# Optimization experiments

Hardware: AMD Instinct MI355X
Metric: run time of the kernel (lower is better)

Reference implementation:

```python
import jax, jax.numpy as jnp
import numpy as np

B, T, E, D, OUT = 512, 128, 256, 256, 1  # batch, steps, enc_hidden, dec_hidden, out_feats


def setup_inputs() -> dict:
    key = jax.random.key(0)
    ks = jax.random.split(key, 16)
    s = lambda k, sh, sc=0.05: jax.random.normal(k, sh, dtype=jnp.float32) * sc
    return {
        "input_encoded": jax.random.normal(ks[0], (B, T, E), dtype=jnp.float32),
        "y_history": jax.random.normal(ks[1], (B, T), dtype=jnp.float32),
        # attn_layer: Linear(2D+E -> E), Tanh, Linear(E -> 1)
        "attn_w1": s(ks[2], (2 * D + E, E)),
        "attn_b1": s(ks[3], (E,)),
        "attn_w2": s(ks[4], (E, 1)),
        "attn_b2": s(ks[5], (1,)),
        # LSTM(out_feats -> D), PyTorch gate order i,f,g,o
        "lstm_w_ih": s(ks[6], (4 * D, OUT)),
        "lstm_w_hh": s(ks[7], (4 * D, D)),
        "lstm_b_ih": s(ks[8], (4 * D,)),
        "lstm_b_hh": s(ks[9], (4 * D,)),
        # fc: Linear(E + out_feats -> out_feats), weight init normal_() in torch
        "fc_w": jax.random.normal(ks[10], (E + OUT, OUT), dtype=jnp.float32),
        "fc_b": s(ks[11], (OUT,)),
        # fc_final: Linear(D + E -> out_feats)
        "fcf_w": s(ks[12], (D + E, OUT)),
        "fcf_b": s(ks[13], (OUT,)),
    }


def _decoder(input_encoded, y_history, attn_w1, attn_b1, attn_w2, attn_b2,
             lstm_w_ih, lstm_w_hh, lstm_b_ih, lstm_b_hh, fc_w, fc_b, fcf_w, fcf_b):
    b, t_steps, e = input_encoded.shape
    d = lstm_w_hh.shape[1]

    def step(carry, y_t):
        h, c, _ = carry  # h,c: [B,D]
        # additive attention over encoder timesteps
        hc = jnp.concatenate([h, c], axis=-1)                      # [B,2D]
        hc_rep = jnp.broadcast_to(hc[:, None, :], (b, t_steps, 2 * d))
        x = jnp.concatenate([hc_rep, input_encoded], axis=-1)      # [B,T,2D+E]
        scores = jnp.tanh(x @ attn_w1 + attn_b1) @ attn_w2 + attn_b2  # [B,T,1]
        attn = jax.nn.softmax(scores[..., 0], axis=1)              # [B,T]
        ctx = jnp.einsum('bt,bte->be', attn, input_encoded)        # [B,E]
        # project (context, y_t) to LSTM input
        y_tilde = jnp.concatenate([ctx, y_t[:, None]], axis=-1) @ fc_w + fc_b  # [B,OUT]
        # one LSTM cell step (gate order i,f,g,o)
        gates = y_tilde @ lstm_w_ih.T + lstm_b_ih + h @ lstm_w_hh.T + lstm_b_hh  # [B,4D]
        i_g, f_g, g_g, o_g = jnp.split(gates, 4, axis=-1)
        c_new = jax.nn.sigmoid(f_g) * c + jax.nn.sigmoid(i_g) * jnp.tanh(g_g)
        h_new = jax.nn.sigmoid(o_g) * jnp.tanh(c_new)
        return (h_new, c_new, ctx), None

    init = (jnp.zeros((b, d), jnp.float32), jnp.zeros((b, d), jnp.float32),
            jnp.zeros((b, e), jnp.float32))
    (h, c, ctx), _ = jax.lax.scan(step, init, y_history.T)  # scan over T
    return jnp.concatenate([h, ctx], axis=-1) @ fcf_w + fcf_b  # [B,OUT]


def reference(input_encoded, y_history, attn_w1, attn_b1, attn_w2, attn_b2,
              lstm_w_ih, lstm_w_hh, lstm_b_ih, lstm_b_hh, fc_w, fc_b, fcf_w, fcf_b):
    return _decoder(input_encoded, y_history, attn_w1, attn_b1, attn_w2, attn_b2,
                    lstm_w_ih, lstm_w_hh, lstm_b_ih, lstm_b_hh, fc_w, fc_b, fcf_w, fcf_b)
```

## Files before the change

### kernel.cpp

```cpp
#include <hip/hip_runtime.h>
#include <hip/hip_bf16.h>

#define NT 128
#define NE 256
#define ND 256

__device__ __forceinline__ float fast_tanh(float x) {
    const float e = __expf(2.f * x);
    return __builtin_fmaf(-2.f, __fdividef(1.f, e + 1.f), 1.f);
}
__device__ __forceinline__ float fast_sigm(float x) {
    return __fdividef(1.f, 1.f + __expf(-x));
}
__device__ __forceinline__ void fma4(float4& a, float s, const float4 b) {
    a.x += s * b.x; a.y += s * b.y; a.z += s * b.z; a.w += s * b.w;
}
__device__ __forceinline__ unsigned short f2bf(float f) {
    unsigned int u = __float_as_uint(f);
    return (unsigned short)((u + 0x7FFFu + ((u >> 16) & 1u)) >> 16);
}
__device__ __forceinline__ float4 unpk(uint2 u) {
    float4 r;
    r.x = __uint_as_float(u.x << 16);
    r.y = __uint_as_float(u.x & 0xFFFF0000u);
    r.z = __uint_as_float(u.y << 16);
    r.w = __uint_as_float(u.y & 0xFFFF0000u);
    return r;
}
__device__ __forceinline__ uint2 pk4(float4 v) {
    uint2 u;
    u.x = (unsigned int)f2bf(v.x) | ((unsigned int)f2bf(v.y) << 16);
    u.y = (unsigned int)f2bf(v.z) | ((unsigned int)f2bf(v.w) << 16);
    return u;
}

__global__ __launch_bounds__(256) void prep_w1_bias(
    const float* __restrict__ w1, const float* __restrict__ bih,
    const float* __restrict__ bhh, unsigned short* __restrict__ w1bf,
    float* __restrict__ biasg)
{
    const int t = threadIdx.x, blk = blockIdx.x;
    if (blk < 512) {
        const int idx = blk * 256 + t;
        w1bf[idx] = f2bf(w1[idx]);
    } else {
        for (int g = t; g < 1024; g += 256) biasg[g] = bih[g] + bhh[g];
    }
}

__global__ __launch_bounds__(256) void transpose_whh_bf(
    const float* __restrict__ whh, unsigned short* __restrict__ whhT)
{
    __shared__ float tile[64][65];
    const int t = threadIdx.x;
    const int bi = blockIdx.x >> 2;
    const int bj = blockIdx.x & 3;
    #pragma unroll
    for (int k = 0; k < 16; ++k) {
        const int idx = k * 256 + t, r = idx >> 6, c = idx & 63;
        tile[r][c] = whh[(size_t)(bi * 64 + r) * 256 + bj * 64 + c];
    }
    __syncthreads();
    #pragma unroll
    for (int k = 0; k < 16; ++k) {
        const int idx = k * 256 + t, r = idx >> 6, c = idx & 63;
        whhT[(size_t)(bj * 64 + r) * 1024 + bi * 64 + c] = f2bf(tile[c][r]);
    }
}

__global__ __launch_bounds__(256) void pre_enc_kernel(
    const float* __restrict__ enc, const float* __restrict__ w1,
    const float* __restrict__ b1, unsigned short* __restrict__ prebf)
{
    __shared__ __align__(16) float encs[8][256];
    const int t = threadIdx.x;
    const size_t r0 = (size_t)blockIdx.x * 8;
    for (int k = t; k < 512; k += 256) {
        const int rl = k >> 6, i4 = (k & 63) * 4;
        *(float4*)&encs[rl][i4] = *(const float4*)(enc + (r0 + rl) * 256 + i4);
    }
    __syncthreads();
    const int rl = t >> 5;
    const int j0 = (t & 31) * 8;
    float4 a0 = *(const float4*)(b1 + j0);
    float4 a1 = *(const float4*)(b1 + j0 + 4);
    const float* wp = w1 + (size_t)512 * 256 + j0;
    #pragma unroll 2
    for (int i = 0; i < 256; i += 4) {
        const float4 e4 = *(const float4*)&encs[rl][i];
        const float* w_i = wp + (size_t)i * 256;
        float4 wa, wb;
        wa = *(const float4*)(w_i);        wb = *(const float4*)(w_i + 4);
        fma4(a0, e4.x, wa); fma4(a1, e4.x, wb);
        wa = *(const float4*)(w_i + 256);  wb = *(const float4*)(w_i + 260);
        fma4(a0, e4.y, wa); fma4(a1, e4.y, wb);
        wa = *(const float4*)(w_i + 512);  wb = *(const float4*)(w_i + 516);
        fma4(a0, e4.z, wa); fma4(a1, e4.z, wb);
        wa = *(const float4*)(w_i + 768);  wb = *(const float4*)(w_i + 772);
        fma4(a0, e4.w, wa); fma4(a1, e4.w, wb);
    }
    unsigned short* op = prebf + (r0 + rl) * 256 + j0;
    const uint2 u0 = pk4(a0), u1 = pk4(a1);
    *(uint2*)op = u0;
    *(uint2*)(op + 4) = u1;
}

__global__ __launch_bounds__(1024) void decoder_main(
    const float* __restrict__ enc, const float* __restrict__ yhist,
    const unsigned short* __restrict__ prebf,
    const unsigned short* __restrict__ w1bf,
    const float* __restrict__ w2g, const unsigned short* __restrict__ whhT,
    const float* __restrict__ wih, const float* __restrict__ biasg,
    const float* __restrict__ fcw, const float* __restrict__ fcb,
    const float* __restrict__ fcfw, const float* __restrict__ fcfb,
    float* __restrict__ out)
{
    __shared__ __align__(16) unsigned short encs[2][128][256];
    __shared__ __align__(16) float part[4096];
    __shared__ __align__(16) float hc2[512][2];
    __shared__ __align__(16) float prehc[2][256];
    __shared__ __align__(16) float scores[2][128];
    __shared__ __align__(16) float ctx[2][256];
    __shared__ __align__(16) float w2s[256];
    __shared__ __align__(16) float fcws[258];
    __shared__ __align__(16) float ys[2][128];
    __shared__ float red[16];
    __shared__ float ytil[2];

    const int t = threadIdx.x;
    const int lane = t & 63;
    const int wv = t >> 6;
    const int b0 = blockIdx.x * 2;

    ((float*)hc2)[t] = 0.f;
    if (t < 256) w2s[t] = w2g[t];
    if (t < 258) fcws[t] = (t < 257) ? fcw[t] : fcb[0];
    if (t < 256) ys[t >> 7][t & 127] = yhist[(size_t)(b0 + (t >> 7)) * NT + (t & 127)];
    #pragma unroll
    for (int k = 0; k < 16; ++k) {
        const int idx = t + k * 1024;
        const int r = idx >> 13, row = (idx >> 6) & 127, eg = idx & 63;
        const float4 v = *(const float4*)(enc + ((size_t)(b0 + r) * NT + row) * NE + eg * 4);
        *(uint2*)&encs[r][row][eg * 4] = pk4(v);
    }
    const int s_ = t >> 3, jc = t & 7;
    const unsigned short* ppre = prebf + ((size_t)b0 * NT + s_) * NE + jc * 4;
    __syncthreads();

    #pragma unroll 1
    for (int ts = 0; ts < NT; ++ts) {
        {
            const int jg = wv & 1;
            const int ib = ((wv >> 1) << 6) + ((lane >> 5) << 5);
            const int jl = (lane & 31) * 4;
            float4 a0 = {0,0,0,0}, a1 = {0,0,0,0};
            const unsigned short* wp = w1bf + (size_t)ib * 256 + jg * 128 + jl;
            #pragma unroll 4
            for (int i = 0; i < 32; ++i) {
                const float4 w4 = unpk(*(const uint2*)(wp + (size_t)i * 256));
                const float2 h2 = *(const float2*)&hc2[ib + i][0];
                fma4(a0, h2.x, w4);
                fma4(a1, h2.y, w4);
            }
            a0.x += __shfl_xor(a0.x, 32); a0.y += __shfl_xor(a0.y, 32);
            a0.z += __shfl_xor(a0.z, 32); a0.w += __shfl_xor(a0.w, 32);
            a1.x += __shfl_xor(a1.x, 32); a1.y += __shfl_xor(a1.y, 32);
            a1.z += __shfl_xor(a1.z, 32); a1.w += __shfl_xor(a1.w, 32);
            if (lane < 32) {
                *(float4*)&part[wv * 256 + jl]       = a0;
                *(float4*)&part[wv * 256 + 128 + jl] = a1;
            }
        }
        __syncthreads();
        if (t < 512) {
            const int r = t >> 8, j = t & 255, jg = j >> 7, jl = j & 127;
            float s = 0.f;
            #pragma unroll
            for (int k = 0; k < 8; ++k) s += part[(2 * k + jg) * 256 + r * 128 + jl];
            prehc[r][j] = s;
        }
        __syncthreads();

        {
            const unsigned short* pp0 = ppre;
            asm volatile("" : "+v"(pp0));
            const unsigned short* pp1 = pp0 + (size_t)NT * NE;
            float a0 = 0.f, a1 = 0.f;
            #pragma unroll
            for (int i = 0; i < 8; ++i) {
                const int j = i * 32 + jc * 4;
                const float4 wv4 = *(const float4*)&w2s[j];
                const float4 h0 = *(const float4*)&prehc[0][j];
                const float4 h1 = *(const float4*)&prehc[1][j];
                const float4 q0 = unpk(*(const uint2*)(pp0 + i * 32));
                const float4 q1 = unpk(*(const uint2*)(pp1 + i * 32));
                a0 += fast_tanh(q0.x + h0.x) * wv4.x + fast_tanh(q0.y + h0.y) * wv4.y
                    + fast_tanh(q0.z + h0.z) * wv4.z + fast_tanh(q0.w + h0.w) * wv4.w;
                a1 += fast_tanh(q1.x + h1.x) * wv4.x + fast_tanh(q1.y + h1.y) * wv4.y
                    + fast_tanh(q1.z + h1.z) * wv4.z + fast_tanh(q1.w + h1.w) * wv4.w;
            }
            a0 += __shfl_xor(a0, 1); a0 += __shfl_xor(a0, 2); a0 += __shfl_xor(a0, 4);
            a1 += __shfl_xor(a1, 1); a1 += __shfl_xor(a1, 2); a1 += __shfl_xor(a1, 4);
            if (jc == 0) { scores[0][s_] = a0; scores[1][s_] = a1; }
        }
        __syncthreads();

        if (t < 128) {
            const int r = t >> 6, l = t & 63;
            const float v0 = scores[r][l], v1 = scores[r][l + 64];
            float m = fmaxf(v0, v1);
            #pragma unroll
            for (int off = 32; off; off >>= 1) m = fmaxf(m, __shfl_xor(m, off));
            const float e0 = __expf(v0 - m), e1 = __expf(v1 - m);
            float sum = e0 + e1;
            #pragma unroll
            for (int off = 32; off; off >>= 1) sum += __shfl_xor(sum, off);
            const float inv = __fdividef(1.f, sum);
            scores[r][l] = e0 * inv;
            scores[r][l + 64] = e1 * inv;
        }
        __syncthreads();

        {
            const int r2 = t >> 9, sl = (t >> 6) & 7, e4 = (t & 63) * 4;
            float4 acc = {0.f, 0.f, 0.f, 0.f};
            #pragma unroll
            for (int q = 0; q < 16; ++q) {
                const float a = scores[r2][sl * 16 + q];
                const uint2 ev = *(const uint2*)&encs[r2][sl * 16 + q][e4];
                fma4(acc, a, unpk(ev));
            }
            *(float4*)&part[(sl * 2 + r2) * 256 + e4] = acc;
        }
        __syncthreads();
        if (t < 512) {
            const int r = t >> 8, e = t & 255;
            float v = 0.f;
            #pragma unroll
            for (int sl2 = 0; sl2 < 8; ++sl2) v += part[(sl2 * 2 + r) * 256 + e];
            ctx[r][e] = v;
            float p = v * fcws[e];
            #pragma unroll
            for (int off = 32; off; off >>= 1) p += __shfl_xor(p, off);
            if (lane == 0) red[wv] = p;
        }
        __syncthreads();

        {
            if (t < 2)
                ytil[t] = red[4 * t] + red[4 * t + 1] + red[4 * t + 2] + red[4 * t + 3]
                        + ys[t][ts] * fcws[256] + fcws[257];
            const int ks = wv >> 3;
            const int cg = wv & 7;
            const int ibase = ks * 128 + (lane >> 5) * 64;
            const int col = cg * 128 + (lane & 31) * 4;
            float4 c0 = {0,0,0,0}, c1 = {0,0,0,0};
            const unsigned short* wp = whhT + (size_t)ibase * 1024 + col;
            #pragma unroll 8
            for (int i = 0; i < 64; ++i) {
                const float4 w4 = unpk(*(const uint2*)(wp + (size_t)i * 1024));
                const float2 h2 = *(const float2*)&hc2[ibase + i][0];
                fma4(c0, h2.x, w4);
                fma4(c1, h2.y, w4);
            }
            c0.x += __shfl_xor(c0.x, 32); c0.y += __shfl_xor(c0.y, 32);
            c0.z += __shfl_xor(c0.z, 32); c0.w += __shfl_xor(c0.w, 32);
            c1.x += __shfl_xor(c1.x, 32); c1.y += __shfl_xor(c1.y, 32);
            c1.z += __shfl_xor(c1.z, 32); c1.w += __shfl_xor(c1.w, 32);
            if (lane < 32) {
                *(float4*)&part[ks * 2048 + col]        = c0;
                *(float4*)&part[ks * 2048 + 1024 + col] = c1;
            }
        }
        __syncthreads();
        if (t < 512) {
            const int r = t >> 8, d = t & 255;
            const float g0 = part[r * 1024 + d]       + part[2048 + r * 1024 + d];
            const float g1 = part[r * 1024 + 256 + d] + part[2048 + r * 1024 + 256 + d];
            const float g2 = part[r * 1024 + 512 + d] + part[2048 + r * 1024 + 512 + d];
            const float g3 = part[r * 1024 + 768 + d] + part[2048 + r * 1024 + 768 + d];
            const float yt = ytil[r];
            const float gi = g0 + yt * wih[d]       + biasg[d];
            const float gf = g1 + yt * wih[256 + d] + biasg[256 + d];
            const float gg = g2 + yt * wih[512 + d] + biasg[512 + d];
            const float go = g3 + yt * wih[768 + d] + biasg[768 + d];
            const float c_old = hc2[256 + d][r];
            const float cn = fast_sigm(gf) * c_old + fast_sigm(gi) * fast_tanh(gg);
            const float hn = fast_sigm(go) * fast_tanh(cn);
            hc2[d][r] = hn;
            hc2[256 + d][r] = cn;
        }
        __syncthreads();
    }

    if (t < 512) {
        const int r = t >> 8, j = t & 255;
        float p = hc2[j][r] * fcfw[j] + ctx[r][j] * fcfw[256 + j];
        #pragma unroll
        for (int off = 32; off; off >>= 1) p += __shfl_xor(p, off);
        if (lane == 0) red[wv] = p;
    }
    __syncthreads();
    if (t < 2)
        out[b0 + t] = red[4 * t] + red[4 * t + 1] + red[4 * t + 2] + red[4 * t + 3] + fcfb[0];
}

extern "C" void kernel_launch(void* const* d_in, const int* in_sizes, int n_in,
                              void* d_out, int out_size, void* d_ws, size_t ws_size,
                              hipStream_t stream) {
    (void)in_sizes; (void)n_in; (void)out_size; (void)ws_size;
    const float* enc   = (const float*)d_in[0];
    const float* yhist = (const float*)d_in[1];
    const float* w1    = (const float*)d_in[2];
    const float* b1    = (const float*)d_in[3];
    const float* w2    = (const float*)d_in[4];
    const float* wih   = (const float*)d_in[6];
    const float* whh   = (const float*)d_in[7];
    const float* bih   = (const float*)d_in[8];
    const float* bhh   = (const float*)d_in[9];
    const float* fcw   = (const float*)d_in[10];
    const float* fcb   = (const float*)d_in[11];
    const float* fcfw  = (const float*)d_in[12];
    const float* fcfb  = (const float*)d_in[13];
    float* out = (float*)d_out;

    unsigned short* prebf = (unsigned short*)d_ws;
    unsigned short* w1bf  = prebf + 16777216;
    unsigned short* whhT  = w1bf + 131072;
    float* biasg = (float*)(whhT + 262144);

    prep_w1_bias<<<513, 256, 0, stream>>>(w1, bih, bhh, w1bf, biasg);
    transpose_whh_bf<<<64, 256, 0, stream>>>(whh, whhT);
    pre_enc_kernel<<<8192, 256, 0, stream>>>(enc, w1, b1, prebf);
    decoder_main<<<256, 1024, 0, stream>>>(enc, yhist, prebf, w1bf, w2, whhT,
                                           wih, biasg, fcw, fcb, fcfw, fcfb, out);
}
```

Measured before the change: 3.718 ms.

## Use bf16 MFMA for per-step hc·W1 and h·Whh matvecs

Replaces the scalar FMA matvecs for the attention hidden-state projection and the LSTM recurrent gates with 16x16x32 bf16 MFMA instructions. Only 2 of the 16 A-matrix rows carry real batch rows; the rest are zeroed. Weights are pre-packed into MFMA fragment layout, and h/c are kept as bf16 in shared memory, with an fp32 copy of c kept for the cell update. This removes the partial-sum reduction pass and one barrier per step. In exchange, most of each MFMA's work is wasted on zero rows, and rounding h/c to bf16 before the matmuls lowers precision.

```diff
diff --git a/kernel.cpp b/kernel.cpp
--- a/kernel.cpp
+++ b/kernel.cpp
@@ -5,6 +5,9 @@
 #define NE 256
 #define ND 256
 
+typedef __attribute__((ext_vector_type(8))) short bf16x8;
+typedef __attribute__((ext_vector_type(4))) float f32x4;
+
 __device__ __forceinline__ float fast_tanh(float x) {
     const float e = __expf(2.f * x);
     return __builtin_fmaf(-2.f, __fdividef(1.f, e + 1.f), 1.f);
@@ -18,6 +21,9 @@
 __device__ __forceinline__ unsigned short f2bf(float f) {
     unsigned int u = __float_as_uint(f);
     return (unsigned short)((u + 0x7FFFu + ((u >> 16) & 1u)) >> 16);
+}
+__device__ __forceinline__ float bf2f(unsigned short s) {
+    return __uint_as_float(((unsigned int)s) << 16);
 }
 __device__ __forceinline__ float4 unpk(uint2 u) {
     float4 r;
@@ -34,37 +40,43 @@
     return u;
 }
 
-__global__ __launch_bounds__(256) void prep_w1_bias(
-    const float* __restrict__ w1, const float* __restrict__ bih,
-    const float* __restrict__ bhh, unsigned short* __restrict__ w1bf,
+__global__ __launch_bounds__(64) void pack_w1mfma(
+    const float* __restrict__ w1, unsigned short* __restrict__ w1m)
+{
+    const int blk = blockIdx.x;
+    const int kt = blk >> 4, nt = blk & 15;
+    const int l = threadIdx.x;
+    const int kb = kt * 32 + (l >> 4) * 8;
+    const int col = nt * 16 + (l & 15);
+    float v[8];
+    #pragma unroll
+    for (int j = 0; j < 8; ++j) v[j] = w1[(size_t)(kb + j) * 256 + col];
+    uint4 o;
+    o.x = (unsigned int)f2bf(v[0]) | ((unsigned int)f2bf(v[1]) << 16);
+    o.y = (unsigned int)f2bf(v[2]) | ((unsigned int)f2bf(v[3]) << 16);
+    o.z = (unsigned int)f2bf(v[4]) | ((unsigned int)f2bf(v[5]) << 16);
+    o.w = (unsigned int)f2bf(v[6]) | ((unsigned int)f2bf(v[7]) << 16);
+    *(uint4*)(w1m + ((size_t)blk * 64 + l) * 8) = o;
+}
+
+__global__ __launch_bounds__(64) void pack_whh_bias(
+    const float* __restrict__ whh, const float* __restrict__ bih,
+    const float* __restrict__ bhh, unsigned short* __restrict__ whhm,
     float* __restrict__ biasg)
 {
-    const int t = threadIdx.x, blk = blockIdx.x;
+    const int blk = blockIdx.x;
+    const int l = threadIdx.x;
     if (blk < 512) {
-        const int idx = blk * 256 + t;
-        w1bf[idx] = f2bf(w1[idx]);
+        const int kt = blk >> 6, nt = blk & 63;
+        const int row = nt * 16 + (l & 15);
+        const int kb = kt * 32 + (l >> 4) * 8;
+        const float4 lo = *(const float4*)&whh[(size_t)row * 256 + kb];
+        const float4 hi = *(const float4*)&whh[(size_t)row * 256 + kb + 4];
+        const uint2 a = pk4(lo), b = pk4(hi);
+        uint4 o; o.x = a.x; o.y = a.y; o.z = b.x; o.w = b.y;
+        *(uint4*)(whhm + ((size_t)blk * 64 + l) * 8) = o;
     } else {
-        for (int g = t; g < 1024; g += 256) biasg[g] = bih[g] + bhh[g];
-    }
-}
-
-__global__ __launch_bounds__(256) void transpose_whh_bf(
-    const float* __restrict__ whh, unsigned short* __restrict__ whhT)
-{
-    __shared__ float tile[64][65];
-    const int t = threadIdx.x;
-    const int bi = blockIdx.x >> 2;
-    const int bj = blockIdx.x & 3;
-    #pragma unroll
-    for (int k = 0; k < 16; ++k) {
-        const int idx = k * 256 + t, r = idx >> 6, c = idx & 63;
-        tile[r][c] = whh[(size_t)(bi * 64 + r) * 256 + bj * 64 + c];
-    }
-    __syncthreads();
-    #pragma unroll
-    for (int k = 0; k < 16; ++k) {
-        const int idx = k * 256 + t, r = idx >> 6, c = idx & 63;
-        whhT[(size_t)(bj * 64 + r) * 1024 + bi * 64 + c] = f2bf(tile[c][r]);
+        for (int g = l; g < 1024; g += 64) biasg[g] = bih[g] + bhh[g];
     }
 }
 
@@ -108,8 +120,8 @@
 __global__ __launch_bounds__(1024) void decoder_main(
     const float* __restrict__ enc, const float* __restrict__ yhist,
     const unsigned short* __restrict__ prebf,
-    const unsigned short* __restrict__ w1bf,
-    const float* __restrict__ w2g, const unsigned short* __restrict__ whhT,
+    const unsigned short* __restrict__ w1m,
+    const float* __restrict__ w2g, const unsigned short* __restrict__ whhm,
     const float* __restrict__ wih, const float* __restrict__ biasg,
     const float* __restrict__ fcw, const float* __restrict__ fcb,
     const float* __restrict__ fcfw, const float* __restrict__ fcfb,
@@ -117,7 +129,8 @@
 {
     __shared__ __align__(16) unsigned short encs[2][128][256];
     __shared__ __align__(16) float part[4096];
-    __shared__ __align__(16) float hc2[512][2];
+    __shared__ __align__(16) unsigned short hcbf[2][512];
+    __shared__ __align__(16) float cfs[2][256];
     __shared__ __align__(16) float prehc[2][256];
     __shared__ __align__(16) float scores[2][128];
     __shared__ __align__(16) float ctx[2][256];
@@ -132,7 +145,7 @@
     const int wv = t >> 6;
     const int b0 = blockIdx.x * 2;
 
-    ((float*)hc2)[t] = 0.f;
+    if (t < 512) { ((unsigned int*)hcbf)[t] = 0u; ((float*)cfs)[t] = 0.f; }
     if (t < 256) w2s[t] = w2g[t];
     if (t < 258) fcws[t] = (t < 257) ? fcw[t] : fcb[0];
     if (t < 256) ys[t >> 7][t & 127] = yhist[(size_t)(b0 + (t >> 7)) * NT + (t & 127)];
@@ -145,39 +158,29 @@
     }
     const int s_ = t >> 3, jc = t & 7;
     const unsigned short* ppre = prebf + ((size_t)b0 * NT + s_) * NE + jc * 4;
+    const int arow = lane & 15;
+    const bool realrow = arow < 2;
+    const int aoff = (lane >> 4) * 8;
+    const bf16x8* w1m8 = (const bf16x8*)w1m;
+    const bf16x8* whm8 = (const bf16x8*)whhm;
+    const bf16x8 azero = {0, 0, 0, 0, 0, 0, 0, 0};
     __syncthreads();
 
     #pragma unroll 1
     for (int ts = 0; ts < NT; ++ts) {
         {
-            const int jg = wv & 1;
-            const int ib = ((wv >> 1) << 6) + ((lane >> 5) << 5);
-            const int jl = (lane & 31) * 4;
-            float4 a0 = {0,0,0,0}, a1 = {0,0,0,0};
-            const unsigned short* wp = w1bf + (size_t)ib * 256 + jg * 128 + jl;
+            f32x4 acc = {0.f, 0.f, 0.f, 0.f};
             #pragma unroll 4
-            for (int i = 0; i < 32; ++i) {
-                const float4 w4 = unpk(*(const uint2*)(wp + (size_t)i * 256));
-                const float2 h2 = *(const float2*)&hc2[ib + i][0];
-                fma4(a0, h2.x, w4);
-                fma4(a1, h2.y, w4);
-            }
-            a0.x += __shfl_xor(a0.x, 32); a0.y += __shfl_xor(a0.y, 32);
-            a0.z += __shfl_xor(a0.z, 32); a0.w += __shfl_xor(a0.w, 32);
-            a1.x += __shfl_xor(a1.x, 32); a1.y += __shfl_xor(a1.y, 32);
-            a1.z += __shfl_xor(a1.z, 32); a1.w += __shfl_xor(a1.w, 32);
-            if (lane < 32) {
-                *(float4*)&part[wv * 256 + jl]       = a0;
-                *(float4*)&part[wv * 256 + 128 + jl] = a1;
-            }
-        }
-        __syncthreads();
-        if (t < 512) {
-            const int r = t >> 8, j = t & 255, jg = j >> 7, jl = j & 127;
-            float s = 0.f;
-            #pragma unroll
-            for (int k = 0; k < 8; ++k) s += part[(2 * k + jg) * 256 + r * 128 + jl];
-            prehc[r][j] = s;
+            for (int kt = 0; kt < 16; ++kt) {
+                bf16x8 a = *(const bf16x8*)&hcbf[arow & 1][kt * 32 + aoff];
+                if (!realrow) a = azero;
+                const bf16x8 b = w1m8[(kt * 16 + wv) * 64 + lane];
+                acc = __builtin_amdgcn_mfma_f32_16x16x32_bf16(a, b, acc, 0, 0, 0);
+            }
+            if (lane < 16) {
+                prehc[0][wv * 16 + lane] = acc[0];
+                prehc[1][wv * 16 + lane] = acc[1];
+            }
         }
         __syncthreads();
 
@@ -250,52 +253,52 @@
             if (t < 2)
                 ytil[t] = red[4 * t] + red[4 * t + 1] + red[4 * t + 2] + red[4 * t + 3]
                         + ys[t][ts] * fcws[256] + fcws[257];
-            const int ks = wv >> 3;
-            const int cg = wv & 7;
-            const int ibase = ks * 128 + (lane >> 5) * 64;
-            const int col = cg * 128 + (lane & 31) * 4;
-            float4 c0 = {0,0,0,0}, c1 = {0,0,0,0};
-            const unsigned short* wp = whhT + (size_t)ibase * 1024 + col;
-            #pragma unroll 8
-            for (int i = 0; i < 64; ++i) {
-                const float4 w4 = unpk(*(const uint2*)(wp + (size_t)i * 1024));
-                const float2 h2 = *(const float2*)&hc2[ibase + i][0];
-                fma4(c0, h2.x, w4);
-                fma4(c1, h2.y, w4);
-            }
-            c0.x += __shfl_xor(c0.x, 32); c0.y += __shfl_xor(c0.y, 32);
-            c0.z += __shfl_xor(c0.z, 32); c0.w += __shfl_xor(c0.w, 32);
-            c1.x += __shfl_xor(c1.x, 32); c1.y += __shfl_xor(c1.y, 32);
-            c1.z += __shfl_xor(c1.z, 32); c1.w += __shfl_xor(c1.w, 32);
-            if (lane < 32) {
-                *(float4*)&part[ks * 2048 + col]        = c0;
-                *(float4*)&part[ks * 2048 + 1024 + col] = c1;
+            f32x4 e0 = {0.f,0.f,0.f,0.f}, e1 = {0.f,0.f,0.f,0.f};
+            f32x4 e2 = {0.f,0.f,0.f,0.f}, e3 = {0.f,0.f,0.f,0.f};
+            #pragma unroll 2
+            for (int kt = 0; kt < 8; ++kt) {
+                bf16x8 a = *(const bf16x8*)&hcbf[arow & 1][kt * 32 + aoff];
+                if (!realrow) a = azero;
+                const int base = (kt * 64 + wv * 4) * 64 + lane;
+                const bf16x8 bq0 = whm8[base];
+                const bf16x8 bq1 = whm8[base + 64];
+                const bf16x8 bq2 = whm8[base + 128];
+                const bf16x8 bq3 = whm8[base + 192];
+                e0 = __builtin_amdgcn_mfma_f32_16x16x32_bf16(a, bq0, e0, 0, 0, 0);
+                e1 = __builtin_amdgcn_mfma_f32_16x16x32_bf16(a, bq1, e1, 0, 0, 0);
+                e2 = __builtin_amdgcn_mfma_f32_16x16x32_bf16(a, bq2, e2, 0, 0, 0);
+                e3 = __builtin_amdgcn_mfma_f32_16x16x32_bf16(a, bq3, e3, 0, 0, 0);
+            }
+            if (lane < 16) {
+                const int nb = wv * 64 + lane;
+                part[nb]           = e0[0]; part[1024 + nb]      = e0[1];
+                part[nb + 16]      = e1[0]; part[1024 + nb + 16] = e1[1];
+                part[nb + 32]      = e2[0]; part[1024 + nb + 32] = e2[1];
+                part[nb + 48]      = e3[0]; part[1024 + nb + 48] = e3[1];
             }
         }
         __syncthreads();
         if (t < 512) {
             const int r = t >> 8, d = t & 255;
-            const float g0 = part[r * 1024 + d]       + part[2048 + r * 1024 + d];
-            const float g1 = part[r * 1024 + 256 + d] + part[2048 + r * 1024 + 256 + d];
-            const float g2 = part[r * 1024 + 512 + d] + part[2048 + r * 1024 + 512 + d];
-            const float g3 = part[r * 1024 + 768 + d] + part[2048 + r * 1024 + 768 + d];
+            const int gb = r * 1024;
             const float yt = ytil[r];
-            const float gi = g0 + yt * wih[d]       + biasg[d];
-            const float gf = g1 + yt * wih[256 + d] + biasg[256 + d];
-            const float gg = g2 + yt * wih[512 + d] + biasg[512 + d];
-            const float go = g3 + yt * wih[768 + d] + biasg[768 + d];
-            const float c_old = hc2[256 + d][r];
+            const float gi = part[gb + d]       + yt * wih[d]       + biasg[d];
+            const float gf = part[gb + 256 + d] + yt * wih[256 + d] + biasg[256 + d];
+            const float gg = part[gb + 512 + d] + yt * wih[512 + d] + biasg[512 + d];
+            const float go = part[gb + 768 + d] + yt * wih[768 + d] + biasg[768 + d];
+            const float c_old = cfs[r][d];
             const float cn = fast_sigm(gf) * c_old + fast_sigm(gi) * fast_tanh(gg);
             const float hn = fast_sigm(go) * fast_tanh(cn);
-            hc2[d][r] = hn;
-            hc2[256 + d][r] = cn;
+            cfs[r][d] = cn;
+            hcbf[r][d] = f2bf(hn);
+            hcbf[r][256 + d] = f2bf(cn);
         }
         __syncthreads();
     }
 
     if (t < 512) {
         const int r = t >> 8, j = t & 255;
-        float p = hc2[j][r] * fcfw[j] + ctx[r][j] * fcfw[256 + j];
+        float p = bf2f(hcbf[r][j]) * fcfw[j] + ctx[r][j] * fcfw[256 + j];
         #pragma unroll
         for (int off = 32; off; off >>= 1) p += __shfl_xor(p, off);
         if (lane == 0) red[wv] = p;
@@ -325,13 +328,13 @@
     float* out = (float*)d_out;
 
     unsigned short* prebf = (unsigned short*)d_ws;
-    unsigned short* w1bf  = prebf + 16777216;
-    unsigned short* whhT  = w1bf + 131072;
-    float* biasg = (float*)(whhT + 262144);
-
-    prep_w1_bias<<<513, 256, 0, stream>>>(w1, bih, bhh, w1bf, biasg);
-    transpose_whh_bf<<<64, 256, 0, stream>>>(whh, whhT);
+    unsigned short* w1m   = prebf + 16777216;
+    unsigned short* whhm  = w1m + 131072;
+    float* biasg = (float*)(whhm + 262144);
+
+    pack_w1mfma<<<256, 64, 0, stream>>>(w1, w1m);
+    pack_whh_bias<<<513, 64, 0, stream>>>(whh, bih, bhh, whhm, biasg);
     pre_enc_kernel<<<8192, 256, 0, stream>>>(enc, w1, b1, prebf);
-    decoder_main<<<256, 1024, 0, stream>>>(enc, yhist, prebf, w1bf, w2, whhT,
+    decoder_main<<<256, 1024, 0, stream>>>(enc, yhist, prebf, w1m, w2, whhm,
                                            wih, biasg, fcw, fcb, fcfw, fcfb, out);
 }
```

Measured after the change: 3.171 ms. -14.7%, faster.
